# Performance work log

Measured on AMD Instinct MI355X. Metric: run time of the kernel, lower is better.

The kernel has to match this reference:

```python
import jax, jax.numpy as jnp
import numpy as np

QMIN, QMAX = 0.0, 255.0
# activation statistics (min, max) per layer, from init_kwargs['stats']
STATS = {"conv1": (-0.5, 3.0), "conv2": (0.0, 6.0), "fc1": (0.0, 8.0), "fc2": (0.0, 10.0)}


def calc_scale_zp(min_val, max_val):
    scale = (max_val - min_val) / (QMAX - QMIN)
    # original: int(clamped initial zero point) -> truncation
    zp = jnp.trunc(jnp.clip(QMIN - min_val / scale, QMIN, QMAX))
    return scale, zp


def quantize(x, min_val=None, max_val=None):
    if min_val is None:
        min_val, max_val = x.min(), x.max()
    scale, zp = calc_scale_zp(min_val, max_val)
    q = jnp.round(jnp.clip(zp + x / scale, QMIN, QMAX))
    return q, scale, zp


def conv2d(x, w, b):
    y = jax.lax.conv_general_dilated(x, w, (1, 1), "VALID",
                                     dimension_numbers=("NCHW", "OIHW", "NCHW"))
    return y + b[None, :, None, None]


def linear(x, w, b):
    return x @ w.T + b


def max_pool_2x2(x):
    return jax.lax.reduce_window(x, -jnp.inf, jax.lax.max, (1, 1, 2, 2), (1, 1, 2, 2), "VALID")


def quantize_layer(q_x, scale_x, zp_x, W, B, apply_fn, stat):
    # fake-quant weights/bias with their own min/max
    wq, scale_w, zp_w = quantize(W)
    bq, scale_b, zp_b = quantize(B)
    scale_next, zp_next = calc_scale_zp(stat[0], stat[1])
    X = q_x - zp_x
    W_eff = scale_x * scale_w * (wq - zp_w)
    B_eff = scale_b * (bq + zp_b)  # '+ zp_b' is faithful to the source
    y = jax.nn.relu(apply_fn(X, W_eff, B_eff) / scale_next + zp_next)
    # .round().byte() in torch wraps mod 256
    return jnp.mod(jnp.round(y), 256.0), scale_next, zp_next


def setup_inputs() -> dict:
    key = jax.random.key(0)
    ks = jax.random.split(key, 9)
    B = 4096
    return {
        "x": jax.random.normal(ks[0], (B, 1, 28, 28), jnp.float32),
        "conv1_w": jax.random.normal(ks[1], (20, 1, 5, 5), jnp.float32) * 0.1,
        "conv1_b": jax.random.normal(ks[2], (20,), jnp.float32) * 0.1,
        "conv2_w": jax.random.normal(ks[3], (50, 20, 5, 5), jnp.float32) * 0.05,
        "conv2_b": jax.random.normal(ks[4], (50,), jnp.float32) * 0.05,
        "fc1_w": jax.random.normal(ks[5], (500, 800), jnp.float32) * 0.03,
        "fc1_b": jax.random.normal(ks[6], (500,), jnp.float32) * 0.03,
        "fc2_w": jax.random.normal(ks[7], (10, 500), jnp.float32) * 0.05,
        "fc2_b": jax.random.normal(ks[8], (10,), jnp.float32) * 0.05,
    }


def reference(x, conv1_w, conv1_b, conv2_w, conv2_b, fc1_w, fc1_b, fc2_w, fc2_b):
    q, s, zp = quantize(x, STATS["conv1"][0], STATS["conv1"][1])
    q, s, zp = quantize_layer(q, s, zp, conv1_w, conv1_b, conv2d, STATS["conv2"])
    q = max_pool_2x2(q)                       # [B,20,12,12]
    q, s, zp = quantize_layer(q, s, zp, conv2_w, conv2_b, conv2d, STATS["fc1"])
    q = max_pool_2x2(q)                       # [B,50,4,4]
    q = q.reshape(-1, 4 * 4 * 50)             # [B,800]
    q, s, zp = quantize_layer(q, s, zp, fc1_w, fc1_b, linear, STATS["fc2"])
    xf = s * (q - zp)                         # dequantize
    logits = linear(xf, fc2_w, fc2_b)         # [B,10]
    return jax.nn.log_softmax(logits, axis=1)
```

## Files before the change

### kernel.cpp

```cpp
#include <hip/hip_runtime.h>
#include <cmath>

#define TPB 256
typedef float floatx4 __attribute__((ext_vector_type(4)));
typedef __bf16 bf16x8 __attribute__((ext_vector_type(8)));
typedef unsigned short ushort8 __attribute__((ext_vector_type(8)));
typedef unsigned short ushort_t;

#define OFF_PMN 16
#define OFF_PMX 96
#define OFF_B1 520
#define OFF_B2 544
#define OFF_B3 600
#define W1BF_BYTE 6144
#define W2BF_BYTE 8192
#define W3BF_BYTE 131072
#define Q2_BYTE  29360128ULL
#define Q3_BYTE  1048576ULL

#define S_X1 (3.5f/255.0f)
#define ZP_X1 36.0f
#define S_N1 (6.0f/255.0f)
#define S_N2 (8.0f/255.0f)
#define S_N3 (10.0f/255.0f)

#define XSTR 40

__device__ inline float qclip(float x, float s, float zp){
    return rintf(fminf(fmaxf(zp + x / s, 0.0f), 255.0f));
}
__device__ inline ushort_t bfbits(float v){
    return (ushort_t)(__float_as_uint(v) >> 16);
}

__global__ __launch_bounds__(TPB) void k_minmax(
        const float* c1w, const float* c1b, const float* c2w, const float* c2b,
        const float* f1w, const float* f1b, float* pmn, float* pmx){
    __shared__ float smn[TPB], smx[TPB];
    int bb = blockIdx.x, tid = threadIdx.x;
    const float* src; int n, sub, nsub;
    if      (bb == 0){ src=c1w; n=500;    sub=0;     nsub=1;  }
    else if (bb == 1){ src=c1b; n=20;     sub=0;     nsub=1;  }
    else if (bb <  6){ src=c2w; n=25000;  sub=bb-2;  nsub=4;  }
    else if (bb == 6){ src=c2b; n=50;     sub=0;     nsub=1;  }
    else if (bb < 71){ src=f1w; n=400000; sub=bb-7;  nsub=64; }
    else             { src=f1b; n=500;    sub=0;     nsub=1;  }
    float mn = INFINITY, mx = -INFINITY;
    for (int i = sub*TPB + tid; i < n; i += nsub*TPB){
        float v = src[i]; mn = fminf(mn, v); mx = fmaxf(mx, v);
    }
    smn[tid] = mn; smx[tid] = mx; __syncthreads();
    for (int s = TPB/2; s > 0; s >>= 1){
        if (tid < s){
            smn[tid] = fminf(smn[tid], smn[tid+s]);
            smx[tid] = fmaxf(smx[tid], smx[tid+s]);
        }
        __syncthreads();
    }
    if (tid == 0){ pmn[bb] = smn[0]; pmx[bb] = smx[0]; }
}

#define N_EFF 452157
__global__ __launch_bounds__(TPB) void k_make_eff(
        const float* c1w, const float* c1b, const float* c2w, const float* c2b,
        const float* f1w, const float* f1b, const float* pmn, const float* pmx,
        float* ws, ushort_t* w1bf, ushort_t* w2bf, ushort_t* w3bf){
    __shared__ float sS[6], sZ[6];
    int tid = threadIdx.x;
    int wv = tid >> 6, lane = tid & 63;
    const int starts[6] = {0,1,2,6,7,71};
    const int counts[6] = {1,1,4,1,64,1};
    #pragma unroll
    for (int rep = 0; rep < 2; ++rep){
        int t = wv + rep*4;
        if (t < 6){
            float mn = INFINITY, mx = -INFINITY;
            if (lane < counts[t]){ mn = pmn[starts[t]+lane]; mx = pmx[starts[t]+lane]; }
            #pragma unroll
            for (int off = 32; off > 0; off >>= 1){
                mn = fminf(mn, __shfl_xor(mn, off));
                mx = fmaxf(mx, __shfl_xor(mx, off));
            }
            if (lane == 0){
                float s = (mx - mn) / 255.0f;
                sS[t] = s;
                sZ[t] = truncf(fminf(fmaxf(0.0f - mn / s, 0.0f), 255.0f));
            }
        }
    }
    __syncthreads();

    int i = blockIdx.x * TPB + tid;
    if (i >= N_EFF) return;
    if (i < 1024){
        int n = i >> 5, k = i & 31;
        float v = 0.0f;
        if (n < 20 && k < 25) v = qclip(c1w[n*25 + k], sS[0], sZ[0]) - sZ[0];
        w1bf[i] = bfbits(v);
    } else if (i < 1044){
        int j = i - 1024;
        ws[OFF_B1 + j] = (sS[1] * (qclip(c1b[j], sS[1], sZ[1]) + sZ[1])) / S_N1;
    } else if (i < 42004){
        int j = i - 1044;
        int c = j >> 11, r = j & 2047, co = r >> 5, k = r & 31;
        int q = k >> 3, jj = k & 7;
        int tap, ci; bool valid;
        if (c < 13){ tap = 2*c + (q>>1); ci = (q&1)*8 + jj; valid = (tap < 25); }
        else       { tap = 4*(c-13) + q; ci = 16 + jj;      valid = (tap < 25) && (jj < 4); }
        valid = valid && (co < 50);
        float v = 0.0f;
        if (valid) v = qclip(c2w[(co*20 + ci)*25 + tap], sS[2], sZ[2]) - sZ[2];
        w2bf[j] = bfbits(v);
    } else if (i < 42054){
        int j = i - 42004;
        ws[OFF_B2 + j] = (sS[3] * (qclip(c2b[j], sS[3], sZ[3]) + sZ[3])) / S_N2;
    } else if (i < 451654){
        int j = i - 42054;
        int n = j / 800, k = j - 800*n;
        float v = 0.0f;
        if (n < 500) v = qclip(f1w[n*800 + k], sS[4], sZ[4]) - sZ[4];
        w3bf[j] = bfbits(v);
    } else if (i < 452154){
        int j = i - 451654;
        ws[OFF_B3 + j] = (sS[5] * (qclip(f1b[j], sS[5], sZ[5]) + sZ[5])) / S_N3;
    } else if (i == 452154){
        ws[0] = (S_N1 * sS[2]) / S_N2;
    } else if (i == 452155){
        ws[1] = (S_N2 * sS[4]) / S_N3;
    } else {
        ws[2] = (S_X1 * sS[0]) / S_N1;
    }
}

__global__ __launch_bounds__(TPB) void k_conv12(const float* x, const ushort_t* w1bf,
                                                const ushort_t* w2bt, const float* ws,
                                                ushort_t* q2bf, int B){
    __shared__ __align__(16) ushort_t xs[144*XSTR];
    __shared__ ushort_t hbu[5760];
    ushort_t* x1 = xs;
    int b = blockIdx.x, tid = threadIdx.x;
    int lane = tid & 63, wv = tid >> 6;
    int ln = lane & 15, quad = lane >> 4;

    const float* xb = x + (size_t)b * 784;
    for (int i = tid; i < 784; i += TPB){
        float v = xb[i];
        float q = rintf(fminf(fmaxf(ZP_X1 + v / S_X1, 0.0f), 255.0f));
        x1[i] = bfbits(q - ZP_X1);
    }

    int offj[8]; bool vj[8];
    #pragma unroll
    for (int j = 0; j < 8; ++j){
        int k = quad*8 + j;
        vj[j] = (k < 25);
        int kh = k / 5, kw = k - 5*kh;
        offj[j] = vj[j] ? (kh*28 + kw) : 0;
    }

    ushort8 bw0 = *(const ushort8*)(w1bf + ln*32 + quad*8);
    ushort8 bw1 = *(const ushort8*)(w1bf + (16 + ln)*32 + quad*8);
    bf16x8 bf0 = __builtin_bit_cast(bf16x8, bw0);
    bf16x8 bf1 = __builtin_bit_cast(bf16x8, bw1);

    float K1 = ws[2];
    float B1_0 = ws[OFF_B1 + ln];
    float B1_1 = (ln < 4) ? ws[OFF_B1 + 16 + ln] : 0.0f;
    __syncthreads();

    for (int i = 0; i < 9; ++i){
        int mt = 9*wv + i;
        int m = mt*16 + ln;
        int oh = m / 24, ow = m - 24*oh;
        int base = oh*28 + ow;
        ushort8 aw;
        #pragma unroll
        for (int j = 0; j < 8; ++j)
            aw[j] = vj[j] ? x1[base + offj[j]] : (ushort_t)0;
        bf16x8 af = __builtin_bit_cast(bf16x8, aw);
        floatx4 z = (floatx4){0.f,0.f,0.f,0.f};
        floatx4 a0 = __builtin_amdgcn_mfma_f32_16x16x32_bf16(af, bf0, z, 0, 0, 0);
        floatx4 a1 = __builtin_amdgcn_mfma_f32_16x16x32_bf16(af, bf1, z, 0, 0, 0);

        int m0 = mt*16 + quad*4;
        int oh0 = m0 / 24, owp = (m0 - 24*oh0) >> 1;
        int hbase = (oh0*12 + owp)*20;
        {
            unsigned int qv[4];
            #pragma unroll
            for (int r = 0; r < 4; ++r){
                float y = fmaxf(fmaf(a0[r], K1, B1_0), 0.0f);
                qv[r] = ((unsigned int)rintf(y)) & 255u;
            }
            unsigned int h0 = qv[0] > qv[1] ? qv[0] : qv[1];
            unsigned int h1 = qv[2] > qv[3] ? qv[2] : qv[3];
            hbu[hbase + ln]      = (ushort_t)h0;
            hbu[hbase + 20 + ln] = (ushort_t)h1;
        }
        if (ln < 4){
            unsigned int qv[4];
            #pragma unroll
            for (int r = 0; r < 4; ++r){
                float y = fmaxf(fmaf(a1[r], K1, B1_1), 0.0f);
                qv[r] = ((unsigned int)rintf(y)) & 255u;
            }
            unsigned int h0 = qv[0] > qv[1] ? qv[0] : qv[1];
            unsigned int h1 = qv[2] > qv[3] ? qv[2] : qv[3];
            hbu[hbase + 16 + ln]      = (ushort_t)h0;
            hbu[hbase + 36 + ln]      = (ushort_t)h1;
        }
    }
    __syncthreads();

    for (int o = tid; o < 3456; o += TPB){
        int p = o / 24, c = o - 24*p;
        unsigned int m_ = 0;
        if (c < 20){
            int ph = p / 12, pw = p - 12*ph;
            unsigned int t_ = hbu[((2*ph)*12 + pw)*20 + c];
            unsigned int u_ = hbu[((2*ph+1)*12 + pw)*20 + c];
            m_ = t_ > u_ ? t_ : u_;
        }
        xs[p*XSTR + c] = bfbits((float)m_);
    }
    __syncthreads();

    int abase[4];
    #pragma unroll
    for (int mt = 0; mt < 4; ++mt)
        abase[mt] = (24*mt + (ln>>3)*12 + (ln&7)) * XSTR;
    int aoff[20];
    #pragma unroll
    for (int c = 0; c < 20; ++c){
        int tap, inner;
        if (c < 13){ tap = 2*c + (quad>>1); inner = (quad&1)*8; }
        else       { tap = 4*(c-13) + quad; inner = 16; }
        int pt = 0;
        if (tap < 25){ int kh = tap/5, kw = tap-5*kh; pt = kh*12 + kw; }
        aoff[c] = pt*XSTR + inner;
    }

    float sc2d = ws[0];
    int co = wv*16 + ln;
    float bias2d = (co < 50) ? ws[OFF_B2 + co] : 0.0f;
    const ushort_t* bsrc = w2bt + (size_t)co*32 + quad*8;

    floatx4 acc[4];
    #pragma unroll
    for (int mt = 0; mt < 4; ++mt) acc[mt] = (floatx4){0.f,0.f,0.f,0.f};

    #pragma unroll
    for (int c = 0; c < 20; ++c){
        ushort8 bw = *(const ushort8*)(bsrc + c*2048);
        bf16x8 bfr = __builtin_bit_cast(bf16x8, bw);
        #pragma unroll
        for (int mt = 0; mt < 4; ++mt){
            ushort8 aw = *(const ushort8*)(xs + abase[mt] + aoff[c]);
            acc[mt] = __builtin_amdgcn_mfma_f32_16x16x32_bf16(
                          __builtin_bit_cast(bf16x8, aw), bfr, acc[mt], 0, 0, 0);
        }
    }

    #pragma unroll
    for (int mt = 0; mt < 4; ++mt){
        unsigned int qv[4];
        #pragma unroll
        for (int r = 0; r < 4; ++r){
            float y = fmaxf(fmaf(acc[mt][r], sc2d, bias2d), 0.0f);
            qv[r] = ((unsigned int)rintf(y)) & 255u;
        }
        unsigned int h0 = qv[0] > qv[1] ? qv[0] : qv[1];
        unsigned int h1 = qv[2] > qv[3] ? qv[2] : qv[3];
        unsigned int p0 = (unsigned int)__shfl_xor((int)h0, 32);
        unsigned int p1 = (unsigned int)__shfl_xor((int)h1, 32);
        unsigned int v0 = h0 > p0 ? h0 : p0;
        unsigned int v1 = h1 > p1 ? h1 : p1;
        if (quad < 2 && co < 50){
            size_t base = (size_t)b*800 + co*16 + mt*4 + quad*2;
            q2bf[base]     = bfbits((float)v0);
            q2bf[base + 1] = bfbits((float)v1);
        }
    }
}

__global__ __launch_bounds__(TPB) void k_fc1(const ushort_t* q2bf, const ushort_t* w3bf,
                                             const float* ws, unsigned char* q3, int B){
    __shared__ ushort_t As[2][64*40];
    int tid = threadIdx.x;
    int n0b = blockIdx.x * 64;
    int b0  = blockIdx.y * 64;
    int lane = tid & 63, wv = tid >> 6;
    int ln = lane & 15, quad = lane >> 4;
    int n0 = n0b + wv*16;
    int lrow = tid >> 2, lk = (tid & 3) * 8;
    const ushort_t* asrc = q2bf + (size_t)(b0 + lrow)*800 + lk;
    ushort_t* adst0 = &As[0][0] + lrow*40 + lk;
    ushort_t* adst1 = &As[1][0] + lrow*40 + lk;

    floatx4 acc[4];
    #pragma unroll
    for (int mt = 0; mt < 4; ++mt) acc[mt] = (floatx4){0.f,0.f,0.f,0.f};

    *(ushort8*)adst0 = *(const ushort8*)asrc;
    __syncthreads();

    for (int c = 0; c < 25; ++c){
        const ushort_t* cur = &As[c & 1][0];
        ushort8 tn;
        bool pf = (c + 1 < 25);
        if (pf) tn = *(const ushort8*)(asrc + (c + 1)*32);
        ushort8 bw = *(const ushort8*)(w3bf + (size_t)(n0 + ln)*800 + c*32 + quad*8);
        bf16x8 bfr = __builtin_bit_cast(bf16x8, bw);
        #pragma unroll
        for (int mt = 0; mt < 4; ++mt){
            ushort8 aw = *(const ushort8*)(cur + (16*mt + ln)*40 + quad*8);
            acc[mt] = __builtin_amdgcn_mfma_f32_16x16x32_bf16(
                          __builtin_bit_cast(bf16x8, aw), bfr, acc[mt], 0, 0, 0);
        }
        if (pf) *(ushort8*)(((c + 1) & 1) ? adst1 : adst0) = tn;
        __syncthreads();
    }

    float sc3d = ws[1];
    int n = n0 + ln;
    if (n < 500){
        float bias = ws[OFF_B3 + n];
        #pragma unroll
        for (int mt = 0; mt < 4; ++mt){
            #pragma unroll
            for (int r = 0; r < 4; ++r){
                int m = 16*mt + 4*quad + r;
                float y = fmaxf(fmaf(acc[mt][r], sc3d, bias), 0.0f);
                q3[(size_t)(b0 + m)*500 + n] = (unsigned char)(((unsigned int)rintf(y)) & 255u);
            }
        }
    }
}

__global__ __launch_bounds__(TPB) void k_fc2(const unsigned char* q3, const float* w2,
                                             const float* b2, float* out, int B){
    __shared__ float w2s[5000];
    __shared__ float b2s[10];
    int tid = threadIdx.x;
    for (int i = tid; i < 5000; i += TPB) w2s[i] = w2[i];
    if (tid < 10) b2s[tid] = b2[tid];
    __syncthreads();
    int lane = tid & 63, wv = tid >> 6;
    for (int rr = 0; rr < 4; ++rr){
        int b = blockIdx.x*16 + wv*4 + rr;
        if (b >= B) break;
        float acc[10];
        #pragma unroll
        for (int c = 0; c < 10; ++c) acc[c] = 0.0f;
        for (int k = lane; k < 500; k += 64){
            float xf = S_N3 * (float)q3[(size_t)b*500 + k];
            #pragma unroll
            for (int c = 0; c < 10; ++c)
                acc[c] = fmaf(xf, w2s[c*500 + k], acc[c]);
        }
        #pragma unroll
        for (int off = 32; off > 0; off >>= 1)
            #pragma unroll
            for (int c = 0; c < 10; ++c)
                acc[c] += __shfl_xor(acc[c], off);
        float lg[10], m = -INFINITY;
        #pragma unroll
        for (int c = 0; c < 10; ++c){ lg[c] = acc[c] + b2s[c]; m = fmaxf(m, lg[c]); }
        float sum = 0.0f;
        #pragma unroll
        for (int c = 0; c < 10; ++c) sum += expf(lg[c] - m);
        float ls = logf(sum);
        if (lane < 10) out[(size_t)b*10 + lane] = lg[lane] - m - ls;
    }
}

extern "C" void kernel_launch(void* const* d_in, const int* in_sizes, int n_in,
                              void* d_out, int out_size, void* d_ws, size_t ws_size,
                              hipStream_t stream){
    const float* x   = (const float*)d_in[0];
    const float* c1w = (const float*)d_in[1];
    const float* c1b = (const float*)d_in[2];
    const float* c2w = (const float*)d_in[3];
    const float* c2b = (const float*)d_in[4];
    const float* f1w = (const float*)d_in[5];
    const float* f1b = (const float*)d_in[6];
    const float* f2w = (const float*)d_in[7];
    const float* f2b = (const float*)d_in[8];
    int B = in_sizes[0] / 784;

    float* ws = (float*)d_ws;
    float* pmn = ws + OFF_PMN;
    float* pmx = ws + OFF_PMX;
    ushort_t* w1bf = (ushort_t*)((char*)d_ws + W1BF_BYTE);
    ushort_t* w2bf = (ushort_t*)((char*)d_ws + W2BF_BYTE);
    ushort_t* w3bf = (ushort_t*)((char*)d_ws + W3BF_BYTE);
    ushort_t* q2bf = (ushort_t*)((char*)d_ws + Q2_BYTE);
    unsigned char* q3 = (unsigned char*)d_ws + Q3_BYTE;
    float* out = (float*)d_out;

    k_minmax<<<72, TPB, 0, stream>>>(c1w, c1b, c2w, c2b, f1w, f1b, pmn, pmx);
    k_make_eff<<<(N_EFF + TPB - 1)/TPB, TPB, 0, stream>>>(c1w, c1b, c2w, c2b, f1w, f1b, pmn, pmx, ws, w1bf, w2bf, w3bf);
    k_conv12<<<B, TPB, 0, stream>>>(x, w1bf, w2bf, ws, q2bf, B);
    dim3 g_fc1(8, B/64);
    k_fc1<<<g_fc1, TPB, 0, stream>>>(q2bf, w3bf, ws, q3, B);
    k_fc2<<<(B + 15)/16, TPB, 0, stream>>>(q3, f2w, f2b, out, B);
}
```

Baseline: 175.9 us.

## Tile conv2 MFMA as 2x2 per wave and replicate conv1 input per quad

The conv2 MFMA work is retiled so each wave computes a 2x2 block of M and N tiles instead of one N tile across four M tiles. This halves the shared-memory A-fragment reads per MFMA while doubling the global weight loads per wave. The conv1 input image is also written four times into shared memory, so each lane quad reads its own copy and LDS bank conflicts on the gather drop. The cost is more shared-memory stores and a larger footprint in xs, which must fit 4*784 elements.

```diff
diff --git a/kernel.cpp b/kernel.cpp
--- a/kernel.cpp
+++ b/kernel.cpp
@@ -137,7 +137,7 @@
                                                 ushort_t* q2bf, int B){
     __shared__ __align__(16) ushort_t xs[144*XSTR];
     __shared__ ushort_t hbu[5760];
-    ushort_t* x1 = xs;
+    ushort_t* xim = xs;
     int b = blockIdx.x, tid = threadIdx.x;
     int lane = tid & 63, wv = tid >> 6;
     int ln = lane & 15, quad = lane >> 4;
@@ -146,7 +146,8 @@
     for (int i = tid; i < 784; i += TPB){
         float v = xb[i];
         float q = rintf(fminf(fmaxf(ZP_X1 + v / S_X1, 0.0f), 255.0f));
-        x1[i] = bfbits(q - ZP_X1);
+        ushort_t bits = bfbits(q - ZP_X1);
+        xim[i] = bits; xim[784 + i] = bits; xim[1568 + i] = bits; xim[2352 + i] = bits;
     }
 
     int offj[8]; bool vj[8];
@@ -157,6 +158,7 @@
         int kh = k / 5, kw = k - 5*kh;
         offj[j] = vj[j] ? (kh*28 + kw) : 0;
     }
+    const ushort_t* xq = xim + quad*784;
 
     ushort8 bw0 = *(const ushort8*)(w1bf + ln*32 + quad*8);
     ushort8 bw1 = *(const ushort8*)(w1bf + (16 + ln)*32 + quad*8);
@@ -176,7 +178,7 @@
         ushort8 aw;
         #pragma unroll
         for (int j = 0; j < 8; ++j)
-            aw[j] = vj[j] ? x1[base + offj[j]] : (ushort_t)0;
+            aw[j] = vj[j] ? xq[base + offj[j]] : (ushort_t)0;
         bf16x8 af = __builtin_bit_cast(bf16x8, aw);
         floatx4 z = (floatx4){0.f,0.f,0.f,0.f};
         floatx4 a0 = __builtin_amdgcn_mfma_f32_16x16x32_bf16(af, bf0, z, 0, 0, 0);
@@ -225,10 +227,12 @@
     }
     __syncthreads();
 
-    int abase[4];
-    #pragma unroll
-    for (int mt = 0; mt < 4; ++mt)
-        abase[mt] = (24*mt + (ln>>3)*12 + (ln&7)) * XSTR;
+    int mt0 = (wv & 1) * 2;
+    int nt0 = (wv >> 1) * 2;
+    int abase[2];
+    #pragma unroll
+    for (int mi = 0; mi < 2; ++mi)
+        abase[mi] = (24*(mt0+mi) + (ln>>3)*12 + (ln&7)) * XSTR;
     int aoff[20];
     #pragma unroll
     for (int c = 0; c < 20; ++c){
@@ -241,44 +245,55 @@
     }
 
     float sc2d = ws[0];
-    int co = wv*16 + ln;
-    float bias2d = (co < 50) ? ws[OFF_B2 + co] : 0.0f;
-    const ushort_t* bsrc = w2bt + (size_t)co*32 + quad*8;
-
-    floatx4 acc[4];
-    #pragma unroll
-    for (int mt = 0; mt < 4; ++mt) acc[mt] = (floatx4){0.f,0.f,0.f,0.f};
+    const ushort_t* bsrc0 = w2bt + (size_t)(nt0*16 + ln)*32 + quad*8;
+    const ushort_t* bsrc1 = bsrc0 + 16*32;
+
+    floatx4 acc[2][2];
+    #pragma unroll
+    for (int mi = 0; mi < 2; ++mi)
+        #pragma unroll
+        for (int ni = 0; ni < 2; ++ni) acc[mi][ni] = (floatx4){0.f,0.f,0.f,0.f};
 
     #pragma unroll
     for (int c = 0; c < 20; ++c){
-        ushort8 bw = *(const ushort8*)(bsrc + c*2048);
-        bf16x8 bfr = __builtin_bit_cast(bf16x8, bw);
-        #pragma unroll
-        for (int mt = 0; mt < 4; ++mt){
-            ushort8 aw = *(const ushort8*)(xs + abase[mt] + aoff[c]);
-            acc[mt] = __builtin_amdgcn_mfma_f32_16x16x32_bf16(
-                          __builtin_bit_cast(bf16x8, aw), bfr, acc[mt], 0, 0, 0);
-        }
-    }
-
-    #pragma unroll
-    for (int mt = 0; mt < 4; ++mt){
-        unsigned int qv[4];
-        #pragma unroll
-        for (int r = 0; r < 4; ++r){
-            float y = fmaxf(fmaf(acc[mt][r], sc2d, bias2d), 0.0f);
-            qv[r] = ((unsigned int)rintf(y)) & 255u;
-        }
-        unsigned int h0 = qv[0] > qv[1] ? qv[0] : qv[1];
-        unsigned int h1 = qv[2] > qv[3] ? qv[2] : qv[3];
-        unsigned int p0 = (unsigned int)__shfl_xor((int)h0, 32);
-        unsigned int p1 = (unsigned int)__shfl_xor((int)h1, 32);
-        unsigned int v0 = h0 > p0 ? h0 : p0;
-        unsigned int v1 = h1 > p1 ? h1 : p1;
-        if (quad < 2 && co < 50){
-            size_t base = (size_t)b*800 + co*16 + mt*4 + quad*2;
-            q2bf[base]     = bfbits((float)v0);
-            q2bf[base + 1] = bfbits((float)v1);
+        ushort8 b0w = *(const ushort8*)(bsrc0 + c*2048);
+        ushort8 b1w = *(const ushort8*)(bsrc1 + c*2048);
+        ushort8 a0w = *(const ushort8*)(xs + abase[0] + aoff[c]);
+        ushort8 a1w = *(const ushort8*)(xs + abase[1] + aoff[c]);
+        bf16x8 a0 = __builtin_bit_cast(bf16x8, a0w);
+        bf16x8 a1 = __builtin_bit_cast(bf16x8, a1w);
+        bf16x8 b0 = __builtin_bit_cast(bf16x8, b0w);
+        bf16x8 b1 = __builtin_bit_cast(bf16x8, b1w);
+        acc[0][0] = __builtin_amdgcn_mfma_f32_16x16x32_bf16(a0, b0, acc[0][0], 0, 0, 0);
+        acc[0][1] = __builtin_amdgcn_mfma_f32_16x16x32_bf16(a0, b1, acc[0][1], 0, 0, 0);
+        acc[1][0] = __builtin_amdgcn_mfma_f32_16x16x32_bf16(a1, b0, acc[1][0], 0, 0, 0);
+        acc[1][1] = __builtin_amdgcn_mfma_f32_16x16x32_bf16(a1, b1, acc[1][1], 0, 0, 0);
+    }
+
+    #pragma unroll
+    for (int ni = 0; ni < 2; ++ni){
+        int co = (nt0 + ni)*16 + ln;
+        float bias2d = (co < 50) ? ws[OFF_B2 + co] : 0.0f;
+        #pragma unroll
+        for (int mi = 0; mi < 2; ++mi){
+            int mt = mt0 + mi;
+            unsigned int qv[4];
+            #pragma unroll
+            for (int r = 0; r < 4; ++r){
+                float y = fmaxf(fmaf(acc[mi][ni][r], sc2d, bias2d), 0.0f);
+                qv[r] = ((unsigned int)rintf(y)) & 255u;
+            }
+            unsigned int h0 = qv[0] > qv[1] ? qv[0] : qv[1];
+            unsigned int h1 = qv[2] > qv[3] ? qv[2] : qv[3];
+            unsigned int p0 = (unsigned int)__shfl_xor((int)h0, 32);
+            unsigned int p1 = (unsigned int)__shfl_xor((int)h1, 32);
+            unsigned int v0 = h0 > p0 ? h0 : p0;
+            unsigned int v1 = h1 > p1 ? h1 : p1;
+            if (quad < 2 && co < 50){
+                size_t base = (size_t)b*800 + co*16 + mt*4 + quad*2;
+                q2bf[base]     = bfbits((float)v0);
+                q2bf[base + 1] = bfbits((float)v1);
+            }
         }
     }
 }
```

Result: no change. 174.1 us (-1.0%).
